# Optimization experiments

Hardware: AMD Instinct MI355X
Metric: run time of the kernel (lower is better)

## Reference

```python
import jax, jax.numpy as jnp
import numpy as np

N, E, F_IN, H, C = 200000, 6400000, 512, 16, 7


def setup_inputs() -> dict:
    key = jax.random.key(0)
    ks = jax.random.split(key, 10)
    return {
        "x": jax.random.normal(ks[0], (N, F_IN), jnp.float32),
        "edge_attr": jax.random.uniform(ks[1], (E, 1), dtype=jnp.float32),
        "src": jax.random.randint(ks[2], (E,), 0, N),
        "dst": jax.random.randint(ks[3], (E,), 0, N),
        "W1": jax.random.normal(ks[4], (2, F_IN, H), jnp.float32) * 0.05,
        "root1": jax.random.normal(ks[5], (F_IN, H), jnp.float32) * 0.05,
        "bias1": jnp.zeros((H,), jnp.float32),
        "W2": jax.random.normal(ks[6], (2, H, C), jnp.float32) * 0.25,
        "root2": jax.random.normal(ks[7], (H, C), jnp.float32) * 0.25,
        "bias2": jnp.zeros((C,), jnp.float32),
    }


def spline_conv(x, u, src, dst, W, root, bias, n_nodes):
    # 1-D open B-spline, degree 1, kernel_size 2: basis weights (1-u, u)
    b1 = jnp.clip(u[:, 0], 0.0, 1.0)            # [E]
    b0 = 1.0 - b1
    h = jnp.einsum('nf,kfo->kno', x, W)         # [2, N, out] - transform before gather
    msg = h[0][src] * b0[:, None] + h[1][src] * b1[:, None]   # [E, out]
    agg = jax.ops.segment_sum(msg, dst, num_segments=n_nodes)  # [N, out]
    deg = jax.ops.segment_sum(jnp.ones((msg.shape[0],), msg.dtype), dst,
                              num_segments=n_nodes)
    agg = agg / jnp.maximum(deg, 1.0)[:, None]  # mean aggregation (SplineConv default)
    return agg + x @ root + bias


def reference(x, edge_attr, src, dst, W1, root1, bias1, W2, root2, bias2):
    n = x.shape[0]
    # eval mode: dropout is identity
    h = jax.nn.elu(spline_conv(x, edge_attr, src, dst, W1, root1, bias1, n))
    out = spline_conv(h, edge_attr, src, dst, W2, root2, bias2, n)
    return jax.nn.log_softmax(out, axis=1)
```

## Files before the change

### kernel.cpp

```cpp
#include <hip/hip_runtime.h>
#include <hip/hip_fp16.h>
#include <math.h>

#define N_NODES 200000
#define N_EDGES 6400000
#define F_INF   512
#define HID     16
#define NCLS    7

#define NPB      1024
#define NBUCKET  ((N_NODES + NPB - 1) / NPB)
#define CHUNK    16384
#define NBLKE    ((N_EDGES + CHUNK - 1) / CHUNK)

#define GROWS 64
#define KCHG  256
#define ASTR  264

typedef _Float16 f16x8 __attribute__((ext_vector_type(8)));
typedef float    f32x4 __attribute__((ext_vector_type(4)));

__global__ __launch_bounds__(256) void packB_kernel(
    const float* __restrict__ W1, const float* __restrict__ root1,
    __half* __restrict__ Bf) {
    int tt = blockIdx.x * 256 + threadIdx.x;
    if (tt >= 3 * 16 * 64) return;
    int lane = tt & 63, kk = (tt >> 6) & 15, t = tt >> 10;
    int col = lane & 15;
    int kbase = kk * 32 + (lane >> 4) * 8;
    const float* __restrict__ srcm = (t == 0) ? W1
                                   : (t == 1) ? (W1 + F_INF * HID) : root1;
    #pragma unroll
    for (int j = 0; j < 8; ++j)
        Bf[(size_t)tt * 8 + j] = __float2half(srcm[(kbase + j) * HID + col]);
}

__global__ __launch_bounds__(256) void gemm1_kernel(
    const float* __restrict__ x, const __half* __restrict__ Bf,
    __half2* __restrict__ hbufH, __half* __restrict__ rbufH) {
    __shared__ __half As[GROWS * ASTR];
    int tid = threadIdx.x;
    int l = tid & 63, w = tid >> 6;
    int rowBase = blockIdx.x * GROWS;

    f32x4 acc0 = {0.f, 0.f, 0.f, 0.f};
    f32x4 acc1 = {0.f, 0.f, 0.f, 0.f};
    f32x4 acc2 = {0.f, 0.f, 0.f, 0.f};

    const __half* __restrict__ Arow = &As[(w * 16 + (l & 15)) * ASTR + (l >> 4) * 8];

    for (int ch = 0; ch < F_INF / KCHG; ++ch) {
        __syncthreads();
        #pragma unroll
        for (int j = 0; j < 16; ++j) {
            int row = w * 16 + j;
            float4 v = *(const float4*)(x + (size_t)(rowBase + row) * F_INF
                                          + ch * KCHG + l * 4);
            union { __half2 h2[2]; float2 f2; } u;
            u.h2[0] = __floats2half2_rn(v.x, v.y);
            u.h2[1] = __floats2half2_rn(v.z, v.w);
            *(float2*)(&As[row * ASTR + l * 4]) = u.f2;
        }
        __syncthreads();
        #pragma unroll
        for (int kkl = 0; kkl < 8; ++kkl) {
            f16x8 a = *(const f16x8*)(Arow + kkl * 32);
            int kkg = ch * 8 + kkl;
            const __half* bp = Bf + ((size_t)kkg * 64 + l) * 8;
            f16x8 b0 = *(const f16x8*)(bp);
            f16x8 b1 = *(const f16x8*)(bp + 16 * 64 * 8);
            f16x8 b2 = *(const f16x8*)(bp + 2 * 16 * 64 * 8);
            acc0 = __builtin_amdgcn_mfma_f32_16x16x32_f16(a, b0, acc0, 0, 0, 0);
            acc1 = __builtin_amdgcn_mfma_f32_16x16x32_f16(a, b1, acc1, 0, 0, 0);
            acc2 = __builtin_amdgcn_mfma_f32_16x16x32_f16(a, b2, acc2, 0, 0, 0);
        }
    }
    int c = l & 15;
    int rbase = rowBase + w * 16 + (l >> 4) * 4;
    #pragma unroll
    for (int r = 0; r < 4; ++r) {
        int n = rbase + r;
        hbufH[(size_t)n * HID + c] = __floats2half2_rn(acc0[r], acc1[r]);
        rbufH[(size_t)n * HID + c] = __float2half(acc2[r]);
    }
}

__global__ __launch_bounds__(256) void p1_bincount(const int* __restrict__ dst,
                                                   int* __restrict__ blockOff) {
    __shared__ int hist[4][NBUCKET];
    int tid = threadIdx.x, w = tid >> 6;
    for (int i = tid; i < 4 * NBUCKET; i += 256) hist[i / NBUCKET][i % NBUCKET] = 0;
    __syncthreads();
    size_t base = (size_t)blockIdx.x * CHUNK;
    for (int i = 0; i < CHUNK / 256; ++i) {
        size_t e = base + (size_t)i * 256 + tid;
        if (e < N_EDGES) atomicAdd(&hist[w][dst[e] >> 10], 1);
    }
    __syncthreads();
    for (int i = tid; i < NBUCKET; i += 256)
        blockOff[(size_t)i * NBLKE + blockIdx.x] =
            hist[0][i] + hist[1][i] + hist[2][i] + hist[3][i];
}

__global__ __launch_bounds__(256) void p2a_kernel(int* __restrict__ blockOff,
                                                  int* __restrict__ bucketTotal) {
    __shared__ int wsum[4];
    int b = blockIdx.x, tid = threadIdx.x;
    size_t rowb = (size_t)b * NBLKE;
    int i0 = tid * 2, i1 = i0 + 1;
    int v0 = (i0 < NBLKE) ? blockOff[rowb + i0] : 0;
    int v1 = (i1 < NBLKE) ? blockOff[rowb + i1] : 0;
    int s = v0 + v1;
    int lane = tid & 63, wid = tid >> 6;
    int incl = s;
    #pragma unroll
    for (int o = 1; o < 64; o <<= 1) {
        int t = __shfl_up(incl, o, 64);
        if (lane >= o) incl += t;
    }
    if (lane == 63) wsum[wid] = incl;
    __syncthreads();
    int woff = 0;
    for (int w = 0; w < wid; ++w) woff += wsum[w];
    int excl = woff + incl - s;
    if (i0 < NBLKE) blockOff[rowb + i0] = excl;
    if (i1 < NBLKE) blockOff[rowb + i1] = excl + v0;
    if (tid == 255) bucketTotal[b] = woff + incl;
}

__global__ __launch_bounds__(256) void p2b_kernel(const int* __restrict__ bucketTotal,
                                                  int* __restrict__ bucketStart,
                                                  int* __restrict__ rowptr) {
    __shared__ int wsum[4];
    int tid = threadIdx.x;
    int base = tid * 4;
    int v[4]; int s = 0;
    #pragma unroll
    for (int q = 0; q < 4; ++q) {
        int idx = base + q;
        v[q] = (idx < NBUCKET) ? bucketTotal[idx] : 0;
        s += v[q];
    }
    int lane = tid & 63, wid = tid >> 6;
    int incl = s;
    #pragma unroll
    for (int o = 1; o < 64; o <<= 1) {
        int t = __shfl_up(incl, o, 64);
        if (lane >= o) incl += t;
    }
    if (lane == 63) wsum[wid] = incl;
    __syncthreads();
    int woff = 0;
    for (int w = 0; w < wid; ++w) woff += wsum[w];
    int run = woff + incl - s;
    #pragma unroll
    for (int q = 0; q < 4; ++q) {
        int idx = base + q;
        if (idx < NBUCKET) bucketStart[idx] = run;
        run += v[q];
    }
    if (tid == 0) rowptr[N_NODES] = N_EDGES;
}

__global__ __launch_bounds__(256) void p3_binscatter(
    const int* __restrict__ dst, const int* __restrict__ src,
    const float* __restrict__ eattr,
    const int* __restrict__ blockOff, const int* __restrict__ bucketStart,
    unsigned int* __restrict__ metaArr, __half* __restrict__ wHarr) {
    __shared__ int cur[NBUCKET];
    int tid = threadIdx.x;
    for (int i = tid; i < NBUCKET; i += 256)
        cur[i] = bucketStart[i] + blockOff[(size_t)i * NBLKE + blockIdx.x];
    __syncthreads();
    size_t base = (size_t)blockIdx.x * CHUNK;
    for (int i = 0; i < CHUNK / 256; ++i) {
        size_t e = base + (size_t)i * 256 + tid;
        if (e < N_EDGES) {
            int d = dst[e];
            int b = d >> 10;
            int slot = atomicAdd(&cur[b], 1);
            unsigned int meta = ((unsigned int)(d & 1023) << 18) | (unsigned int)src[e];
            float w = fminf(fmaxf(eattr[e], 0.f), 1.f);
            metaArr[slot] = meta;
            wHarr[slot] = __float2half(w);
        }
    }
}

__global__ __launch_bounds__(1024) void p4_buildcsr(
    const int* __restrict__ bucketStart, const int* __restrict__ bucketTotal,
    const unsigned int* __restrict__ metaArr, const __half* __restrict__ wHarr,
    unsigned int* __restrict__ packedS, int* __restrict__ rowptr) {
    __shared__ int hist[NPB];
    __shared__ int wsum[16];
    int b = blockIdx.x, tid = threadIdx.x;
    int start = bucketStart[b], count = bucketTotal[b];
    int nn = min(NPB, N_NODES - b * NPB);
    hist[tid] = 0;
    __syncthreads();
    for (int i = tid; i < count; i += 1024)
        atomicAdd(&hist[metaArr[start + i] >> 18], 1);
    __syncthreads();
    int v = hist[tid];
    int lane = tid & 63, wid = tid >> 6;
    int incl = v;
    #pragma unroll
    for (int o = 1; o < 64; o <<= 1) {
        int t = __shfl_up(incl, o, 64);
        if (lane >= o) incl += t;
    }
    if (lane == 63) wsum[wid] = incl;
    __syncthreads();
    int woff = 0;
    for (int w = 0; w < wid; ++w) woff += wsum[w];
    int excl = woff + incl - v;
    if (tid < nn) rowptr[b * NPB + tid] = start + excl;
    hist[tid] = excl;
    __syncthreads();
    for (int i = tid; i < count; i += 1024) {
        unsigned int m = metaArr[start + i];
        float w = __half2float(wHarr[start + i]);
        unsigned int wq = (unsigned int)(w * 16383.0f + 0.5f);
        int pos = start + atomicAdd(&hist[m >> 18], 1);
        packedS[pos] = (wq << 18) | (m & 0x3FFFFu);
    }
}

__global__ __launch_bounds__(256) void agg1_kernel(
    const unsigned int* __restrict__ packedS, const int* __restrict__ rowptr,
    const __half2* __restrict__ hbufH, __half* __restrict__ rbufH,
    const float* __restrict__ bias1) {
    int n = blockIdx.x * 4 + (threadIdx.x >> 6);
    if (n >= N_NODES) return;
    int lane = threadIdx.x & 63;
    int c = lane & 15, sub = lane >> 4;
    int beg = rowptr[n], end = rowptr[n + 1];
    float acc = 0.f;
    int p = beg + sub;
    for (; p + 4 < end; p += 8) {
        unsigned int m0 = packedS[p];
        unsigned int m1 = packedS[p + 4];
        float w0 = (float)(m0 >> 18) * (1.0f / 16383.0f);
        float w1 = (float)(m1 >> 18) * (1.0f / 16383.0f);
        float2 h0 = __half22float2(hbufH[(size_t)(m0 & 0x3FFFFu) * HID + c]);
        float2 h1 = __half22float2(hbufH[(size_t)(m1 & 0x3FFFFu) * HID + c]);
        acc += fmaf(w0, h0.y - h0.x, h0.x);
        acc += fmaf(w1, h1.y - h1.x, h1.x);
    }
    if (p < end) {
        unsigned int m = packedS[p];
        float w = (float)(m >> 18) * (1.0f / 16383.0f);
        float2 h = __half22float2(hbufH[(size_t)(m & 0x3FFFFu) * HID + c]);
        acc += fmaf(w, h.y - h.x, h.x);
    }
    acc += __shfl_xor(acc, 16, 64);
    acc += __shfl_xor(acc, 32, 64);
    if (sub == 0) {
        float invd = 1.0f / fmaxf((float)(end - beg), 1.0f);
        float r = __half2float(rbufH[(size_t)n * HID + c]);
        float vv = fmaf(acc, invd, r) + bias1[c];
        float hv = vv > 0.f ? vv : expm1f(vv);
        rbufH[(size_t)n * HID + c] = __float2half(hv);
    }
}

__global__ __launch_bounds__(256) void node1b_kernel(
    const __half* __restrict__ rbufH, const float* __restrict__ W2,
    const float* __restrict__ root2,
    __half2* __restrict__ h2buf, float* __restrict__ r2buf) {
    int n = blockIdx.x * 256 + threadIdx.x;
    if (n >= N_NODES) return;
    float h[HID];
    #pragma unroll
    for (int k = 0; k < HID; ++k) h[k] = __half2float(rbufH[(size_t)n * HID + k]);
    float o0[NCLS], o1[NCLS], orr[NCLS];
    #pragma unroll
    for (int j = 0; j < NCLS; ++j) { o0[j] = 0.f; o1[j] = 0.f; orr[j] = 0.f; }
    const float* __restrict__ W2b = W2 + HID * NCLS;
    #pragma unroll
    for (int k = 0; k < HID; ++k) {
        #pragma unroll
        for (int j = 0; j < NCLS; ++j) {
            o0[j]  = fmaf(h[k], W2 [k * NCLS + j], o0[j]);
            o1[j]  = fmaf(h[k], W2b[k * NCLS + j], o1[j]);
            orr[j] = fmaf(h[k], root2[k * NCLS + j], orr[j]);
        }
    }
    __half2* hb = h2buf + (size_t)n * 8;
    float*   r2 = r2buf + (size_t)n * 8;
    #pragma unroll
    for (int j = 0; j < NCLS; ++j) {
        hb[j] = __floats2half2_rn(o0[j], o1[j]);
        r2[j] = orr[j];
    }
    hb[7] = __floats2half2_rn(0.f, 0.f);
    r2[7] = 0.f;
}

__global__ __launch_bounds__(256) void agg2_kernel(
    const unsigned int* __restrict__ packedS, const int* __restrict__ rowptr,
    const __half2* __restrict__ h2buf, const float* __restrict__ r2buf,
    const float* __restrict__ bias2, float* __restrict__ out) {
    int n = blockIdx.x * 4 + (threadIdx.x >> 6);
    if (n >= N_NODES) return;
    int lane = threadIdx.x & 63;
    int j = lane & 7, sub = lane >> 3;
    int beg = rowptr[n], end = rowptr[n + 1];
    float acc = 0.f;
    int p = beg + sub;
    for (; p + 8 < end; p += 16) {
        unsigned int m0 = packedS[p];
        unsigned int m1 = packedS[p + 8];
        float w0 = (float)(m0 >> 18) * (1.0f / 16383.0f);
        float w1 = (float)(m1 >> 18) * (1.0f / 16383.0f);
        float2 h0 = __half22float2(h2buf[(size_t)(m0 & 0x3FFFFu) * 8 + j]);
        float2 h1 = __half22float2(h2buf[(size_t)(m1 & 0x3FFFFu) * 8 + j]);
        acc += fmaf(w0, h0.y - h0.x, h0.x);
        acc += fmaf(w1, h1.y - h1.x, h1.x);
    }
    if (p < end) {
        unsigned int m = packedS[p];
        float w = (float)(m >> 18) * (1.0f / 16383.0f);
        float2 h = __half22float2(h2buf[(size_t)(m & 0x3FFFFu) * 8 + j]);
        acc += fmaf(w, h.y - h.x, h.x);
    }
    acc += __shfl_xor(acc, 8, 64);
    acc += __shfl_xor(acc, 16, 64);
    acc += __shfl_xor(acc, 32, 64);
    if (sub == 0) {
        float invd = 1.0f / fmaxf((float)(end - beg), 1.0f);
        float v = fmaf(acc, invd, r2buf[(size_t)n * 8 + j]) + ((j < NCLS) ? bias2[j] : 0.f);
        if (j == NCLS) v = -INFINITY;
        float mx = v;
        mx = fmaxf(mx, __shfl_xor(mx, 1, 8));
        mx = fmaxf(mx, __shfl_xor(mx, 2, 8));
        mx = fmaxf(mx, __shfl_xor(mx, 4, 8));
        float ex = expf(v - mx);
        float sm = ex;
        sm += __shfl_xor(sm, 1, 8);
        sm += __shfl_xor(sm, 2, 8);
        sm += __shfl_xor(sm, 4, 8);
        float lse = mx + logf(sm);
        if (j < NCLS) out[(size_t)n * NCLS + j] = v - lse;
    }
}

extern "C" void kernel_launch(void* const* d_in, const int* in_sizes, int n_in,
                              void* d_out, int out_size, void* d_ws, size_t ws_size,
                              hipStream_t stream) {
    const float* x     = (const float*)d_in[0];
    const float* eattr = (const float*)d_in[1];
    const int*   src   = (const int*)d_in[2];
    const int*   dst   = (const int*)d_in[3];
    const float* W1    = (const float*)d_in[4];
    const float* root1 = (const float*)d_in[5];
    const float* bias1 = (const float*)d_in[6];
    const float* W2    = (const float*)d_in[7];
    const float* root2 = (const float*)d_in[8];
    const float* bias2 = (const float*)d_in[9];
    float* out = (float*)d_out;

    char* wp = (char*)d_ws;
    unsigned int* metaArr = (unsigned int*)wp;  wp += (size_t)N_EDGES * 4;
    __half*       wHarr   = (__half*)wp;        wp += (size_t)N_EDGES * 2;
    unsigned int* packedS = (unsigned int*)wp;  wp += (size_t)N_EDGES * 4;
    int* blockOff    = (int*)wp;                wp += (size_t)NBUCKET * NBLKE * 4;
    int* bucketTotal = (int*)wp;                wp += 1024 * 4;
    int* bucketStart = (int*)wp;                wp += 1024 * 4;
    int* rowptr      = (int*)wp;                wp += (size_t)(N_NODES + 4) * 4;
    __half* Bf       = (__half*)wp;             wp += (size_t)3 * 16 * 64 * 8 * 2;
    __half2* hbufH   = (__half2*)wp;            wp += (size_t)N_NODES * HID * 4;
    __half*  rbufH   = (__half*)wp;             wp += (size_t)N_NODES * HID * 2;
    __half2* h2buf = hbufH;
    float*   r2buf = (float*)(hbufH + (size_t)N_NODES * 8);

    const int node_blocks = (N_NODES + 255) / 256;
    const int wave_blocks = (N_NODES + 3) / 4;

    hipLaunchKernelGGL(packB_kernel, dim3((3 * 16 * 64 + 255) / 256), dim3(256), 0, stream,
                       W1, root1, Bf);
    hipLaunchKernelGGL(gemm1_kernel, dim3(N_NODES / GROWS), dim3(256), 0, stream,
                       x, Bf, hbufH, rbufH);
    hipLaunchKernelGGL(p1_bincount, dim3(NBLKE), dim3(256), 0, stream, dst, blockOff);
    hipLaunchKernelGGL(p2a_kernel, dim3(NBUCKET), dim3(256), 0, stream,
                       blockOff, bucketTotal);
    hipLaunchKernelGGL(p2b_kernel, dim3(1), dim3(256), 0, stream,
                       bucketTotal, bucketStart, rowptr);
    hipLaunchKernelGGL(p3_binscatter, dim3(NBLKE), dim3(256), 0, stream,
                       dst, src, eattr, blockOff, bucketStart, metaArr, wHarr);
    hipLaunchKernelGGL(p4_buildcsr, dim3(NBUCKET), dim3(1024), 0, stream,
                       bucketStart, bucketTotal, metaArr, wHarr, packedS, rowptr);
    hipLaunchKernelGGL(agg1_kernel, dim3(wave_blocks), dim3(256), 0, stream,
                       packedS, rowptr, hbufH, rbufH, bias1);
    hipLaunchKernelGGL(node1b_kernel, dim3(node_blocks), dim3(256), 0, stream,
                       rbufH, W2, root2, h2buf, r2buf);
    hipLaunchKernelGGL(agg2_kernel, dim3(wave_blocks), dim3(256), 0, stream,
                       packedS, rowptr, h2buf, r2buf, bias2, out);
}
```

Before: 567.8 us.

## Fuse GEMM with dst bincount, fold layer-2 transform into agg1, unroll gathers

Merges the layer-1 GEMM and the dst histogram pass into one heterogeneous launch, so the two independent workloads can overlap on the GPU. The per-node layer-2 linear transform is moved into the agg1 kernel through a small LDS staging buffer, which removes a separate kernel and the round trip of the hidden features. The edge gather loops in both aggregation kernels are unrolled to four loads per lane to increase memory-level parallelism. In exchange it uses separate h2/r2 buffers and drops the bounds checks, relying on N being divisible by 4.

```diff
diff --git a/kernel.cpp b/kernel.cpp
--- a/kernel.cpp
+++ b/kernel.cpp
@@ -16,6 +16,7 @@
 #define GROWS 64
 #define KCHG  256
 #define ASTR  264
+#define GEMM_BLOCKS (N_NODES / GROWS)
 
 typedef _Float16 f16x8 __attribute__((ext_vector_type(8)));
 typedef float    f32x4 __attribute__((ext_vector_type(4)));
@@ -35,71 +36,74 @@
         Bf[(size_t)tt * 8 + j] = __float2half(srcm[(kbase + j) * HID + col]);
 }
 
-__global__ __launch_bounds__(256) void gemm1_kernel(
+__global__ __launch_bounds__(256) void gemm1p1_kernel(
     const float* __restrict__ x, const __half* __restrict__ Bf,
-    __half2* __restrict__ hbufH, __half* __restrict__ rbufH) {
-    __shared__ __half As[GROWS * ASTR];
+    __half2* __restrict__ hbufH, __half* __restrict__ rbufH,
+    const int* __restrict__ dst, int* __restrict__ blockOff) {
+    __shared__ char smem[GROWS * ASTR * 2];
     int tid = threadIdx.x;
-    int l = tid & 63, w = tid >> 6;
-    int rowBase = blockIdx.x * GROWS;
-
-    f32x4 acc0 = {0.f, 0.f, 0.f, 0.f};
-    f32x4 acc1 = {0.f, 0.f, 0.f, 0.f};
-    f32x4 acc2 = {0.f, 0.f, 0.f, 0.f};
-
-    const __half* __restrict__ Arow = &As[(w * 16 + (l & 15)) * ASTR + (l >> 4) * 8];
-
-    for (int ch = 0; ch < F_INF / KCHG; ++ch) {
+
+    if (blockIdx.x < GEMM_BLOCKS) {
+        __half* As = (__half*)smem;
+        int l = tid & 63, w = tid >> 6;
+        int rowBase = blockIdx.x * GROWS;
+
+        f32x4 acc0 = {0.f, 0.f, 0.f, 0.f};
+        f32x4 acc1 = {0.f, 0.f, 0.f, 0.f};
+        f32x4 acc2 = {0.f, 0.f, 0.f, 0.f};
+
+        const __half* __restrict__ Arow = &As[(w * 16 + (l & 15)) * ASTR + (l >> 4) * 8];
+
+        for (int ch = 0; ch < F_INF / KCHG; ++ch) {
+            __syncthreads();
+            #pragma unroll
+            for (int j = 0; j < 16; ++j) {
+                int row = w * 16 + j;
+                float4 v = *(const float4*)(x + (size_t)(rowBase + row) * F_INF
+                                              + ch * KCHG + l * 4);
+                union { __half2 h2[2]; float2 f2; } u;
+                u.h2[0] = __floats2half2_rn(v.x, v.y);
+                u.h2[1] = __floats2half2_rn(v.z, v.w);
+                *(float2*)(&As[row * ASTR + l * 4]) = u.f2;
+            }
+            __syncthreads();
+            #pragma unroll
+            for (int kkl = 0; kkl < 8; ++kkl) {
+                f16x8 a = *(const f16x8*)(Arow + kkl * 32);
+                int kkg = ch * 8 + kkl;
+                const __half* bp = Bf + ((size_t)kkg * 64 + l) * 8;
+                f16x8 b0 = *(const f16x8*)(bp);
+                f16x8 b1 = *(const f16x8*)(bp + 16 * 64 * 8);
+                f16x8 b2 = *(const f16x8*)(bp + 2 * 16 * 64 * 8);
+                acc0 = __builtin_amdgcn_mfma_f32_16x16x32_f16(a, b0, acc0, 0, 0, 0);
+                acc1 = __builtin_amdgcn_mfma_f32_16x16x32_f16(a, b1, acc1, 0, 0, 0);
+                acc2 = __builtin_amdgcn_mfma_f32_16x16x32_f16(a, b2, acc2, 0, 0, 0);
+            }
+        }
+        int c = l & 15;
+        int rbase = rowBase + w * 16 + (l >> 4) * 4;
+        #pragma unroll
+        for (int r = 0; r < 4; ++r) {
+            int n = rbase + r;
+            hbufH[(size_t)n * HID + c] = __floats2half2_rn(acc0[r], acc1[r]);
+            rbufH[(size_t)n * HID + c] = __float2half(acc2[r]);
+        }
+    } else {
+        int bb = blockIdx.x - GEMM_BLOCKS;
+        int (*hist)[NBUCKET] = (int(*)[NBUCKET])smem;
+        int w = tid >> 6;
+        for (int i = tid; i < 4 * NBUCKET; i += 256) hist[i / NBUCKET][i % NBUCKET] = 0;
         __syncthreads();
-        #pragma unroll
-        for (int j = 0; j < 16; ++j) {
-            int row = w * 16 + j;
-            float4 v = *(const float4*)(x + (size_t)(rowBase + row) * F_INF
-                                          + ch * KCHG + l * 4);
-            union { __half2 h2[2]; float2 f2; } u;
-            u.h2[0] = __floats2half2_rn(v.x, v.y);
-            u.h2[1] = __floats2half2_rn(v.z, v.w);
-            *(float2*)(&As[row * ASTR + l * 4]) = u.f2;
+        size_t base = (size_t)bb * CHUNK;
+        for (int i = 0; i < CHUNK / 256; ++i) {
+            size_t e = base + (size_t)i * 256 + tid;
+            if (e < N_EDGES) atomicAdd(&hist[w][dst[e] >> 10], 1);
         }
         __syncthreads();
-        #pragma unroll
-        for (int kkl = 0; kkl < 8; ++kkl) {
-            f16x8 a = *(const f16x8*)(Arow + kkl * 32);
-            int kkg = ch * 8 + kkl;
-            const __half* bp = Bf + ((size_t)kkg * 64 + l) * 8;
-            f16x8 b0 = *(const f16x8*)(bp);
-            f16x8 b1 = *(const f16x8*)(bp + 16 * 64 * 8);
-            f16x8 b2 = *(const f16x8*)(bp + 2 * 16 * 64 * 8);
-            acc0 = __builtin_amdgcn_mfma_f32_16x16x32_f16(a, b0, acc0, 0, 0, 0);
-            acc1 = __builtin_amdgcn_mfma_f32_16x16x32_f16(a, b1, acc1, 0, 0, 0);
-            acc2 = __builtin_amdgcn_mfma_f32_16x16x32_f16(a, b2, acc2, 0, 0, 0);
-        }
-    }
-    int c = l & 15;
-    int rbase = rowBase + w * 16 + (l >> 4) * 4;
-    #pragma unroll
-    for (int r = 0; r < 4; ++r) {
-        int n = rbase + r;
-        hbufH[(size_t)n * HID + c] = __floats2half2_rn(acc0[r], acc1[r]);
-        rbufH[(size_t)n * HID + c] = __float2half(acc2[r]);
-    }
-}
-
-__global__ __launch_bounds__(256) void p1_bincount(const int* __restrict__ dst,
-                                                   int* __restrict__ blockOff) {
-    __shared__ int hist[4][NBUCKET];
-    int tid = threadIdx.x, w = tid >> 6;
-    for (int i = tid; i < 4 * NBUCKET; i += 256) hist[i / NBUCKET][i % NBUCKET] = 0;
-    __syncthreads();
-    size_t base = (size_t)blockIdx.x * CHUNK;
-    for (int i = 0; i < CHUNK / 256; ++i) {
-        size_t e = base + (size_t)i * 256 + tid;
-        if (e < N_EDGES) atomicAdd(&hist[w][dst[e] >> 10], 1);
-    }
-    __syncthreads();
-    for (int i = tid; i < NBUCKET; i += 256)
-        blockOff[(size_t)i * NBLKE + blockIdx.x] =
-            hist[0][i] + hist[1][i] + hist[2][i] + hist[3][i];
+        for (int i = tid; i < NBUCKET; i += 256)
+            blockOff[(size_t)i * NBLKE + bb] =
+                hist[0][i] + hist[1][i] + hist[2][i] + hist[3][i];
+    }
 }
 
 __global__ __launch_bounds__(256) void p2a_kernel(int* __restrict__ blockOff,
@@ -226,28 +230,39 @@
     }
 }
 
-__global__ __launch_bounds__(256) void agg1_kernel(
+__global__ __launch_bounds__(256) void agg1f_kernel(
     const unsigned int* __restrict__ packedS, const int* __restrict__ rowptr,
-    const __half2* __restrict__ hbufH, __half* __restrict__ rbufH,
-    const float* __restrict__ bias1) {
-    int n = blockIdx.x * 4 + (threadIdx.x >> 6);
-    if (n >= N_NODES) return;
+    const __half2* __restrict__ hbufH, const __half* __restrict__ rbufH,
+    const float* __restrict__ bias1, const float* __restrict__ W2,
+    const float* __restrict__ root2,
+    __half2* __restrict__ h2buf, float* __restrict__ r2buf) {
+    __shared__ float hsh[4][16];
+    int wv = threadIdx.x >> 6;
+    int n = blockIdx.x * 4 + wv;
     int lane = threadIdx.x & 63;
     int c = lane & 15, sub = lane >> 4;
     int beg = rowptr[n], end = rowptr[n + 1];
     float acc = 0.f;
     int p = beg + sub;
-    for (; p + 4 < end; p += 8) {
+    for (; p + 12 < end; p += 16) {
         unsigned int m0 = packedS[p];
         unsigned int m1 = packedS[p + 4];
+        unsigned int m2 = packedS[p + 8];
+        unsigned int m3 = packedS[p + 12];
         float w0 = (float)(m0 >> 18) * (1.0f / 16383.0f);
         float w1 = (float)(m1 >> 18) * (1.0f / 16383.0f);
+        float w2 = (float)(m2 >> 18) * (1.0f / 16383.0f);
+        float w3 = (float)(m3 >> 18) * (1.0f / 16383.0f);
         float2 h0 = __half22float2(hbufH[(size_t)(m0 & 0x3FFFFu) * HID + c]);
         float2 h1 = __half22float2(hbufH[(size_t)(m1 & 0x3FFFFu) * HID + c]);
+        float2 h2 = __half22float2(hbufH[(size_t)(m2 & 0x3FFFFu) * HID + c]);
+        float2 h3 = __half22float2(hbufH[(size_t)(m3 & 0x3FFFFu) * HID + c]);
         acc += fmaf(w0, h0.y - h0.x, h0.x);
         acc += fmaf(w1, h1.y - h1.x, h1.x);
-    }
-    if (p < end) {
+        acc += fmaf(w2, h2.y - h2.x, h2.x);
+        acc += fmaf(w3, h3.y - h3.x, h3.x);
+    }
+    for (; p < end; p += 4) {
         unsigned int m = packedS[p];
         float w = (float)(m >> 18) * (1.0f / 16383.0f);
         float2 h = __half22float2(hbufH[(size_t)(m & 0x3FFFFu) * HID + c]);
@@ -259,42 +274,27 @@
         float invd = 1.0f / fmaxf((float)(end - beg), 1.0f);
         float r = __half2float(rbufH[(size_t)n * HID + c]);
         float vv = fmaf(acc, invd, r) + bias1[c];
-        float hv = vv > 0.f ? vv : expm1f(vv);
-        rbufH[(size_t)n * HID + c] = __float2half(hv);
-    }
-}
-
-__global__ __launch_bounds__(256) void node1b_kernel(
-    const __half* __restrict__ rbufH, const float* __restrict__ W2,
-    const float* __restrict__ root2,
-    __half2* __restrict__ h2buf, float* __restrict__ r2buf) {
-    int n = blockIdx.x * 256 + threadIdx.x;
-    if (n >= N_NODES) return;
-    float h[HID];
-    #pragma unroll
-    for (int k = 0; k < HID; ++k) h[k] = __half2float(rbufH[(size_t)n * HID + k]);
-    float o0[NCLS], o1[NCLS], orr[NCLS];
-    #pragma unroll
-    for (int j = 0; j < NCLS; ++j) { o0[j] = 0.f; o1[j] = 0.f; orr[j] = 0.f; }
-    const float* __restrict__ W2b = W2 + HID * NCLS;
-    #pragma unroll
-    for (int k = 0; k < HID; ++k) {
-        #pragma unroll
-        for (int j = 0; j < NCLS; ++j) {
-            o0[j]  = fmaf(h[k], W2 [k * NCLS + j], o0[j]);
-            o1[j]  = fmaf(h[k], W2b[k * NCLS + j], o1[j]);
-            orr[j] = fmaf(h[k], root2[k * NCLS + j], orr[j]);
+        hsh[wv][c] = vv > 0.f ? vv : expm1f(vv);
+    }
+    if (lane < 8) {
+        int j = lane;
+        if (j < NCLS) {
+            const float* __restrict__ W2b = W2 + HID * NCLS;
+            float o0 = 0.f, o1 = 0.f, orr = 0.f;
+            #pragma unroll
+            for (int k = 0; k < HID; ++k) {
+                float h = hsh[wv][k];
+                o0  = fmaf(h, W2 [k * NCLS + j], o0);
+                o1  = fmaf(h, W2b[k * NCLS + j], o1);
+                orr = fmaf(h, root2[k * NCLS + j], orr);
+            }
+            h2buf[(size_t)n * 8 + j] = __floats2half2_rn(o0, o1);
+            r2buf[(size_t)n * 8 + j] = orr;
+        } else {
+            h2buf[(size_t)n * 8 + 7] = __floats2half2_rn(0.f, 0.f);
+            r2buf[(size_t)n * 8 + 7] = 0.f;
         }
     }
-    __half2* hb = h2buf + (size_t)n * 8;
-    float*   r2 = r2buf + (size_t)n * 8;
-    #pragma unroll
-    for (int j = 0; j < NCLS; ++j) {
-        hb[j] = __floats2half2_rn(o0[j], o1[j]);
-        r2[j] = orr[j];
-    }
-    hb[7] = __floats2half2_rn(0.f, 0.f);
-    r2[7] = 0.f;
 }
 
 __global__ __launch_bounds__(256) void agg2_kernel(
@@ -302,23 +302,30 @@
     const __half2* __restrict__ h2buf, const float* __restrict__ r2buf,
     const float* __restrict__ bias2, float* __restrict__ out) {
     int n = blockIdx.x * 4 + (threadIdx.x >> 6);
-    if (n >= N_NODES) return;
     int lane = threadIdx.x & 63;
     int j = lane & 7, sub = lane >> 3;
     int beg = rowptr[n], end = rowptr[n + 1];
     float acc = 0.f;
     int p = beg + sub;
-    for (; p + 8 < end; p += 16) {
+    for (; p + 24 < end; p += 32) {
         unsigned int m0 = packedS[p];
         unsigned int m1 = packedS[p + 8];
+        unsigned int m2 = packedS[p + 16];
+        unsigned int m3 = packedS[p + 24];
         float w0 = (float)(m0 >> 18) * (1.0f / 16383.0f);
         float w1 = (float)(m1 >> 18) * (1.0f / 16383.0f);
+        float w2 = (float)(m2 >> 18) * (1.0f / 16383.0f);
+        float w3 = (float)(m3 >> 18) * (1.0f / 16383.0f);
         float2 h0 = __half22float2(h2buf[(size_t)(m0 & 0x3FFFFu) * 8 + j]);
         float2 h1 = __half22float2(h2buf[(size_t)(m1 & 0x3FFFFu) * 8 + j]);
+        float2 h2 = __half22float2(h2buf[(size_t)(m2 & 0x3FFFFu) * 8 + j]);
+        float2 h3 = __half22float2(h2buf[(size_t)(m3 & 0x3FFFFu) * 8 + j]);
         acc += fmaf(w0, h0.y - h0.x, h0.x);
         acc += fmaf(w1, h1.y - h1.x, h1.x);
-    }
-    if (p < end) {
+        acc += fmaf(w2, h2.y - h2.x, h2.x);
+        acc += fmaf(w3, h3.y - h3.x, h3.x);
+    }
+    for (; p < end; p += 8) {
         unsigned int m = packedS[p];
         float w = (float)(m >> 18) * (1.0f / 16383.0f);
         float2 h = __half22float2(h2buf[(size_t)(m & 0x3FFFFu) * 8 + j]);
@@ -371,17 +378,15 @@
     __half* Bf       = (__half*)wp;             wp += (size_t)3 * 16 * 64 * 8 * 2;
     __half2* hbufH   = (__half2*)wp;            wp += (size_t)N_NODES * HID * 4;
     __half*  rbufH   = (__half*)wp;             wp += (size_t)N_NODES * HID * 2;
-    __half2* h2buf = hbufH;
-    float*   r2buf = (float*)(hbufH + (size_t)N_NODES * 8);
-
-    const int node_blocks = (N_NODES + 255) / 256;
-    const int wave_blocks = (N_NODES + 3) / 4;
+    __half2* h2buf   = (__half2*)wp;            wp += (size_t)N_NODES * 8 * 4;
+    float*   r2buf   = (float*)wp;              wp += (size_t)N_NODES * 8 * 4;
+
+    const int wave_blocks = N_NODES / 4;
 
     hipLaunchKernelGGL(packB_kernel, dim3((3 * 16 * 64 + 255) / 256), dim3(256), 0, stream,
                        W1, root1, Bf);
-    hipLaunchKernelGGL(gemm1_kernel, dim3(N_NODES / GROWS), dim3(256), 0, stream,
-                       x, Bf, hbufH, rbufH);
-    hipLaunchKernelGGL(p1_bincount, dim3(NBLKE), dim3(256), 0, stream, dst, blockOff);
+    hipLaunchKernelGGL(gemm1p1_kernel, dim3(GEMM_BLOCKS + NBLKE), dim3(256), 0, stream,
+                       x, Bf, hbufH, rbufH, dst, blockOff);
     hipLaunchKernelGGL(p2a_kernel, dim3(NBUCKET), dim3(256), 0, stream,
                        blockOff, bucketTotal);
     hipLaunchKernelGGL(p2b_kernel, dim3(1), dim3(256), 0, stream,
@@ -390,10 +395,8 @@
                        dst, src, eattr, blockOff, bucketStart, metaArr, wHarr);
     hipLaunchKernelGGL(p4_buildcsr, dim3(NBUCKET), dim3(1024), 0, stream,
                        bucketStart, bucketTotal, metaArr, wHarr, packedS, rowptr);
-    hipLaunchKernelGGL(agg1_kernel, dim3(wave_blocks), dim3(256), 0, stream,
-                       packedS, rowptr, hbufH, rbufH, bias1);
-    hipLaunchKernelGGL(node1b_kernel, dim3(node_blocks), dim3(256), 0, stream,
-                       rbufH, W2, root2, h2buf, r2buf);
+    hipLaunchKernelGGL(agg1f_kernel, dim3(wave_blocks), dim3(256), 0, stream,
+                       packedS, rowptr, hbufH, rbufH, bias1, W2, root2, h2buf, r2buf);
     hipLaunchKernelGGL(agg2_kernel, dim3(wave_blocks), dim3(256), 0, stream,
                        packedS, rowptr, h2buf, r2buf, bias2, out);
 }
```

After: 584.7 us. 1.03x slower.
